# Optimization experiments

Measured on AMD Instinct MI355X. Metric: run time of the kernel, lower is better.

The kernel has to match this reference:

```python
import jax, jax.numpy as jnp
import numpy as np

H = 1024
B, S = 4, 2048
SCALE = 1.0 / np.sqrt(H)  # single-head: head_dim == hidden_dim


def setup_inputs() -> dict:
    key = jax.random.key(0)
    k1, k2, k3, k4 = jax.random.split(key, 4)
    inp = jax.random.normal(k1, (B, S, H), dtype=jnp.float32)
    # nn.Linear(h, h, bias=False) weights, stored [out, in]
    wq = jax.random.normal(k2, (H, H), dtype=jnp.float32) / np.sqrt(H)
    wk = jax.random.normal(k3, (H, H), dtype=jnp.float32) / np.sqrt(H)
    wv = jax.random.normal(k4, (H, H), dtype=jnp.float32) / np.sqrt(H)
    # causal mask, broadcast over batch: 1 = attend, 0 = masked
    attention_mask = jnp.broadcast_to(
        jnp.tril(jnp.ones((S, S), dtype=jnp.int32)), (B, S, S))
    return {"input": inp, "attention_mask": attention_mask,
            "wq": wq, "wk": wk, "wv": wv}


def reference(input, attention_mask, wq, wk, wv):
    # Linear: x @ W^T
    Q = jnp.einsum('bsh,oh->bso', input, wq)
    K = jnp.einsum('bsh,oh->bso', input, wk)
    V = jnp.einsum('bsh,oh->bso', input, wv)
    scores = jnp.einsum('bqh,bkh->bqk', Q, K) * SCALE  # [B,S,S]
    neg_inf = jnp.asarray(-jnp.inf, dtype=scores.dtype)
    scores = jnp.where(attention_mask == 0, neg_inf, scores)
    attn = jax.nn.softmax(scores, axis=-1)
    # dropout prob = 0.0 (eval): identity
    return jnp.einsum('bqk,bkh->bqh', attn, V)
```

## Files before the change

### kernel.cpp

```cpp
#include <hip/hip_runtime.h>
#include <hip/hip_bf16.h>
#include <stdint.h>

typedef __attribute__((ext_vector_type(8))) short short8;
typedef __attribute__((ext_vector_type(4))) float f32x4;
typedef __attribute__((ext_vector_type(4))) float fvec4;
typedef __attribute__((ext_vector_type(4))) unsigned short us4;

#define DEV static __device__ __forceinline__

constexpr int Hn = 1024;
constexpr int Bn = 4;
constexpr int Sn = 2048;
constexpr float SCALE_F = 0.03125f;
constexpr float LOG2E_F = 1.4426950408889634f;
constexpr float CEXP = SCALE_F * LOG2E_F;

DEV unsigned short f2bf(float f) {
  union { float f; unsigned u; } c; c.f = f;
  unsigned r = c.u + 0x7fffu + ((c.u >> 16) & 1u);
  return (unsigned short)(r >> 16);
}

DEV float bf2f(unsigned short b) {
  union { unsigned u; float f; } c; c.u = ((unsigned)b) << 16;
  return c.f;
}

DEV void gload16(const void* g, void* l) {
  __builtin_amdgcn_global_load_lds(
      (const __attribute__((address_space(1))) void*)g,
      (__attribute__((address_space(3))) void*)l, 16, 0, 0);
}

DEV void hw_barrier() { asm volatile("s_barrier" ::: "memory"); }

DEV int swz_wg(int bid, int n) {
  const int q = n >> 3, r = n & 7, x = bid & 7, o = bid >> 3;
  return (x < r ? x * (q + 1) : r * (q + 1) + (x - r) * q) + o;
}

__global__ __launch_bounds__(256) void cvt_kernel(
    const float* __restrict__ x, const float* __restrict__ wq,
    const float* __restrict__ wk, const float* __restrict__ wv,
    unsigned short* __restrict__ xb, unsigned short* __restrict__ wb) {
  const int NX4 = Bn * Sn * Hn / 4;
  const int NW4 = Hn * Hn / 4;
  const int total = NX4 + 3 * NW4;
  for (int i = blockIdx.x * 256 + threadIdx.x; i < total; i += gridDim.x * 256) {
    const fvec4* s; us4* d; int j;
    if (i < NX4)                { s = (const fvec4*)x;  d = (us4*)xb;             j = i; }
    else if (i < NX4 + NW4)     { s = (const fvec4*)wq; d = (us4*)wb;             j = i - NX4; }
    else if (i < NX4 + 2 * NW4) { s = (const fvec4*)wk; d = (us4*)(wb + Hn * Hn); j = i - NX4 - NW4; }
    else                        { s = (const fvec4*)wv; d = (us4*)(wb + 2 * Hn * Hn); j = i - NX4 - 2 * NW4; }
    fvec4 v = s[j];
    us4 o;
    o[0] = f2bf(v[0]); o[1] = f2bf(v[1]); o[2] = f2bf(v[2]); o[3] = f2bf(v[3]);
    d[j] = o;
  }
}

template <int MODE>
__global__ __launch_bounds__(512, 2) void gemm256_kernel(
    const unsigned short* __restrict__ A, int lda, int64_t a_bstride,
    const unsigned short* __restrict__ Bm, int ldb, int64_t b_bstride,
    unsigned short* __restrict__ C0, unsigned short* __restrict__ C1,
    int n_split, int ldc, int64_t c_bstride, int bm_mod, int K) {
  __shared__ __attribute__((aligned(16))) unsigned short LA[2][256 * 64];
  __shared__ __attribute__((aligned(16))) unsigned short LB[2][256 * 64];
  const int tid = threadIdx.x, lane = tid & 63, wave = tid >> 6;
  const int wr = wave >> 2, wc = wave & 3;

  int bm, bn;
  const unsigned short* Ab = A;
  const unsigned short* Bb = Bm;
  unsigned short* Cb = C0;
  if (MODE == 0) {
    const int wg = swz_wg(blockIdx.x, gridDim.x);
    bm = wg % bm_mod;
    bn = wg / bm_mod;
  } else {
    const int wg = swz_wg(blockIdx.x, gridDim.x);
    const int zl = wg / 36;
    const int t = wg - zl * 36;
    bm = (int)((sqrtf(8.f * t + 1.f) - 1.f) * 0.5f);
    if (bm * (bm + 1) / 2 > t) bm--;
    if ((bm + 1) * (bm + 2) / 2 <= t) bm++;
    bn = t - bm * (bm + 1) / 2;
    Ab += (int64_t)zl * a_bstride;
    Bb += (int64_t)zl * b_bstride;
    Cb += (int64_t)zl * c_bstride;
  }

  const int srow = wave * 32 + (lane >> 3);
  const int scol = (((lane & 7) ^ (lane >> 3)) << 3);
  const unsigned short* AgS = Ab + (int64_t)(bm * 256 + srow) * lda + scol;
  const unsigned short* BgS = Bb + (int64_t)(bn * 256 + srow) * ldb + scol;

  f32x4 zero = {0.f, 0.f, 0.f, 0.f};
  f32x4 acc[8][4];
#pragma unroll
  for (int m = 0; m < 8; m++)
#pragma unroll
    for (int n = 0; n < 4; n++) acc[m][n] = zero;

  auto stage = [&](int t, int buf) {
    char* la = (char*)LA[buf] + wave * 4096;
    char* lb = (char*)LB[buf] + wave * 4096;
    const int k0 = t << 6;
#pragma unroll
    for (int j = 0; j < 4; ++j) {
      gload16(AgS + (int64_t)(j * 8) * lda + k0, la + j * 1024);
      gload16(BgS + (int64_t)(j * 8) * ldb + k0, lb + j * 1024);
    }
  };

  const int nkt = K >> 6;
  const int ln15 = lane & 15;
  const int hi = (lane >> 4) * 16;
  const int sw = (ln15 & 7) << 4;

  stage(0, 0);
  for (int t = 0; t < nkt; ++t) {
    const int buf = t & 1;
    hw_barrier();
    if (t + 1 < nkt) {
      stage(t + 1, buf ^ 1);
      asm volatile("s_waitcnt vmcnt(8)" ::: "memory");
    } else {
      asm volatile("s_waitcnt vmcnt(0)" ::: "memory");
    }
    hw_barrier();
    __builtin_amdgcn_sched_barrier(0);

    const char* la = (const char*)LA[buf];
    const char* lb = (const char*)LB[buf];
#pragma unroll
    for (int qm = 0; qm < 2; ++qm) {
#pragma unroll
      for (int ks = 0; ks < 2; ++ks) {
        const int kb = (ks * 64 + hi) ^ sw;
        short8 a[4];
#pragma unroll
        for (int fr = 0; fr < 4; ++fr)
          a[fr] = *(const short8*)(la + (wr * 128 + qm * 64 + fr * 16 + ln15) * 128 + kb);
#pragma unroll
        for (int qn = 0; qn < 2; ++qn) {
          short8 b0 = *(const short8*)(lb + (wc * 64 + qn * 32 + ln15) * 128 + kb);
          short8 b1 = *(const short8*)(lb + (wc * 64 + qn * 32 + 16 + ln15) * 128 + kb);
          __builtin_amdgcn_s_setprio(1);
#pragma unroll
          for (int fr = 0; fr < 4; ++fr) {
            acc[qm * 4 + fr][qn * 2 + 0] =
                __builtin_amdgcn_mfma_f32_16x16x32_bf16(a[fr], b0, acc[qm * 4 + fr][qn * 2 + 0], 0, 0, 0);
            acc[qm * 4 + fr][qn * 2 + 1] =
                __builtin_amdgcn_mfma_f32_16x16x32_bf16(a[fr], b1, acc[qm * 4 + fr][qn * 2 + 1], 0, 0, 0);
          }
          __builtin_amdgcn_s_setprio(0);
        }
      }
    }
  }

  if (MODE == 0) {
#pragma unroll
    for (int n = 0; n < 4; n++) {
      int cc = bn * 256 + wc * 64 + n * 16;
      unsigned short* cb = Cb;
      if (cc >= n_split) { cb = C1; cc -= n_split; }
      cc += ln15;
#pragma unroll
      for (int m = 0; m < 8; m++) {
        const int r0 = bm * 256 + wr * 128 + m * 16 + ((lane >> 4) << 2);
#pragma unroll
        for (int j = 0; j < 4; j++)
          cb[(int64_t)(r0 + j) * ldc + cc] = f2bf(acc[m][n][j]);
      }
    }
  } else {
#pragma unroll
    for (int n = 0; n < 4; n++) {
      const int cc = bn * 256 + wc * 64 + n * 16 + ln15;
#pragma unroll
      for (int m = 0; m < 8; m++) {
        const int r0 = bm * 256 + wr * 128 + m * 16 + ((lane >> 4) << 2);
#pragma unroll
        for (int j = 0; j < 4; j++) {
          const int row = r0 + j;
          const float p = (cc <= row) ? __builtin_amdgcn_exp2f(acc[m][n][j] * CEXP) : 0.f;
          Cb[(int64_t)row * ldc + cc] = f2bf(p);
        }
      }
    }
  }
}

__global__ __launch_bounds__(256) void rowsum_kernel(
    const unsigned short* __restrict__ P, float* __restrict__ l, int b0, int nb) {
  const int lane = threadIdx.x & 63, wave = threadIdx.x >> 6;
  const int r = blockIdx.x * 4 + wave;
  if (r >= nb * Sn) return;
  const int bl = r >> 11;
  const int q = r & (Sn - 1);
  const unsigned short* Pr = P + (int64_t)bl * Sn * Sn + (int64_t)q * Sn;
  float s = 0.f;
  for (int base = lane * 8; base < Sn; base += 512) {
    const int rem = q + 1 - base;
    if (rem <= 0) continue;
    short8 v = *(const short8*)(Pr + base);
#pragma unroll
    for (int e = 0; e < 8; ++e)
      if (e < rem) s += bf2f((unsigned short)v[e]);
  }
#pragma unroll
  for (int m = 1; m < 64; m <<= 1) s += __shfl_xor(s, m);
  if (lane == 0) l[(int64_t)(b0 + bl) * Sn + q] = s;
}

__global__ __launch_bounds__(256) void pv_gemm_kernel(
    const unsigned short* __restrict__ P, int64_t p_zstride,
    const unsigned short* __restrict__ VTb,
    const float* __restrict__ l,
    float* __restrict__ Out, int b0, int nb) {
  const int per_bm = 8 * nb;
  const int w = blockIdx.x;
  const int bm = 15 - (w / per_bm);
  const int inner = w - (15 - bm) * per_bm;
  const int bn = inner & 7;
  const int zl = inner >> 3;
  const int b = b0 + zl;

  __shared__ __attribute__((aligned(16))) unsigned short As[2][128 * 32];
  __shared__ __attribute__((aligned(16))) unsigned short Bs[2][128 * 32];
  const int tid = threadIdx.x, lane = tid & 63, wave = tid >> 6;
  const int wr = wave >> 1, wc = wave & 1;

  const unsigned short* A = P + (int64_t)zl * p_zstride;
  const unsigned short* Ag = A + (int64_t)(bm * 128 + wave * 32 + (lane >> 2)) * Sn + (lane & 3) * 8;
  const unsigned short* Bg = VTb + (int64_t)(bn * 128 + wave * 32 + (lane >> 2)) * (Bn * Sn)
                             + (int64_t)b * Sn + (lane & 3) * 8;

  f32x4 zero = {0.f, 0.f, 0.f, 0.f};
  f32x4 acc[4][4];
#pragma unroll
  for (int m = 0; m < 4; m++)
#pragma unroll
    for (int n = 0; n < 4; n++) acc[m][n] = zero;

  auto stage = [&](int kt, int buf) {
    const int k0 = kt << 5;
    char* a = (char*)As[buf] + wave * 2048;
    char* b2 = (char*)Bs[buf] + wave * 2048;
    gload16(Ag + k0, a);
    gload16(Ag + k0 + 16 * Sn, a + 1024);
    gload16(Bg + k0, b2);
    gload16(Bg + k0 + (int64_t)16 * (Bn * Sn), b2 + 1024);
  };

  const int nkt = (bm + 1) * 4;
  stage(0, 0);
  __syncthreads();
  for (int kt = 0; kt < nkt; ++kt) {
    const int buf = kt & 1;
    if (kt + 1 < nkt) stage(kt + 1, buf ^ 1);
    const short* Ap = (const short*)As[buf];
    const short* Bp = (const short*)Bs[buf];
    const int ko = (lane >> 4) * 8;
    short8 af[4], bfv[4];
#pragma unroll
    for (int m = 0; m < 4; m++)
      af[m] = *(const short8*)(Ap + (wr * 64 + m * 16 + (lane & 15)) * 32 + ko);
#pragma unroll
    for (int n = 0; n < 4; n++)
      bfv[n] = *(const short8*)(Bp + (wc * 64 + n * 16 + (lane & 15)) * 32 + ko);
#pragma unroll
    for (int m = 0; m < 4; m++)
#pragma unroll
      for (int n = 0; n < 4; n++)
        acc[m][n] = __builtin_amdgcn_mfma_f32_16x16x32_bf16(af[m], bfv[n], acc[m][n], 0, 0, 0);
    __syncthreads();
  }

#pragma unroll
  for (int m = 0; m < 4; m++) {
    const int r0 = bm * 128 + wr * 64 + m * 16 + ((lane >> 4) << 2);
#pragma unroll
    for (int j = 0; j < 4; j++) {
      const int q = r0 + j;
      const float linv = 1.0f / l[(int64_t)b * Sn + q];
#pragma unroll
      for (int n = 0; n < 4; n++) {
        const int d = bn * 128 + wc * 64 + n * 16 + (lane & 15);
        Out[(int64_t)b * Sn * Hn + (int64_t)q * Hn + d] = acc[m][n][j] * linv;
      }
    }
  }
}

extern "C" void kernel_launch(void* const* d_in, const int* in_sizes, int n_in,
                              void* d_out, int out_size, void* d_ws, size_t ws_size,
                              hipStream_t stream) {
  const float* x  = (const float*)d_in[0];
  const float* wq = (const float*)d_in[2];
  const float* wk = (const float*)d_in[3];
  const float* wv = (const float*)d_in[4];
  float* out = (float*)d_out;
  char* ws = (char*)d_ws;

  const int64_t MiB = 1ll << 20;
  unsigned short* xb = (unsigned short*)(ws);
  unsigned short* wb = (unsigned short*)(ws + 16 * MiB);
  float* l           = (float*)(ws + 22 * MiB);
  unsigned short* Qb = (unsigned short*)(ws + 23 * MiB);
  unsigned short* Kb = (unsigned short*)(ws + 39 * MiB);
  unsigned short* VT = (unsigned short*)(ws + 55 * MiB);
  unsigned short* P  = (unsigned short*)(ws + 71 * MiB);

  cvt_kernel<<<2048, 256, 0, stream>>>(x, wq, wk, wv, xb, wb);
  gemm256_kernel<0><<<256, 512, 0, stream>>>(
      xb, 1024, 0, wb, 1024, 0, Qb, Kb, 1024, 1024, 0, 32, 1024);
  gemm256_kernel<0><<<128, 512, 0, stream>>>(
      wb + 2 * 1024 * 1024, 1024, 0, xb, 1024, 0, VT, VT, 1 << 30, 8192, 0, 4, 1024);

  int nb = 1;
  if (ws_size >= 103ull * MiB) nb = 4;
  else if (ws_size >= 87ull * MiB) nb = 2;
  for (int b0 = 0; b0 < Bn; b0 += nb) {
    gemm256_kernel<1><<<36 * nb, 512, 0, stream>>>(
        Qb + (int64_t)b0 * Sn * Hn, 1024, (int64_t)Sn * Hn,
        Kb + (int64_t)b0 * Sn * Hn, 1024, (int64_t)Sn * Hn,
        P, nullptr, 1 << 30, Sn, (int64_t)Sn * Sn, 8, 1024);
    rowsum_kernel<<<nb * 512, 256, 0, stream>>>(P, l, b0, nb);
    pv_gemm_kernel<<<16 * 8 * nb, 256, 0, stream>>>(
        P, (int64_t)Sn * Sn, VT, l, out, b0, nb);
  }
}
```

Baseline: 181.6 us.

## Fuse row-sum into QK GEMM, pack causal P tiles, restructure GEMM pipeline

The softmax row-sum is now computed in the QK^T epilogue through wave shuffles and atomicAdd, which removes the separate rowsum kernel and its re-read of P. P is stored as packed lower-triangular 128x128 tiles that reuse the freed xb region, so all batches run in a single launch instead of a workspace-dependent loop. The 256x256 GEMM main loop is rewritten to stage and consume A and B in halves with finer-grained barriers and waitcnts, overlapping loads with MFMA. PV loads use an XOR-swizzled LDS layout to reduce bank conflicts. The cost is atomics on the row sums, a zero-init folded into the convert kernel, and more complex synchronisation.

```diff
diff --git a/kernel.cpp b/kernel.cpp
--- a/kernel.cpp
+++ b/kernel.cpp
@@ -15,6 +15,7 @@
 constexpr float SCALE_F = 0.03125f;
 constexpr float LOG2E_F = 1.4426950408889634f;
 constexpr float CEXP = SCALE_F * LOG2E_F;
+constexpr int PTILES = 136;
 
 DEV unsigned short f2bf(float f) {
   union { float f; unsigned u; } c; c.f = f;
@@ -22,18 +23,15 @@
   return (unsigned short)(r >> 16);
 }
 
-DEV float bf2f(unsigned short b) {
-  union { unsigned u; float f; } c; c.u = ((unsigned)b) << 16;
-  return c.f;
-}
-
 DEV void gload16(const void* g, void* l) {
   __builtin_amdgcn_global_load_lds(
       (const __attribute__((address_space(1))) void*)g,
       (__attribute__((address_space(3))) void*)l, 16, 0, 0);
 }
 
-DEV void hw_barrier() { asm volatile("s_barrier" ::: "memory"); }
+#define VMCNT(n) asm volatile("s_waitcnt vmcnt(" #n ")" ::: "memory")
+#define LGKM0()  asm volatile("s_waitcnt lgkmcnt(0)" ::: "memory")
+#define BAR()    asm volatile("s_barrier" ::: "memory")
 
 DEV int swz_wg(int bid, int n) {
   const int q = n >> 3, r = n & 7, x = bid & 7, o = bid >> 3;
@@ -43,7 +41,12 @@
 __global__ __launch_bounds__(256) void cvt_kernel(
     const float* __restrict__ x, const float* __restrict__ wq,
     const float* __restrict__ wk, const float* __restrict__ wv,
-    unsigned short* __restrict__ xb, unsigned short* __restrict__ wb) {
+    unsigned short* __restrict__ xb, unsigned short* __restrict__ wb,
+    float* __restrict__ lz) {
+  if (blockIdx.x == 0) {
+    f32x4 z = {0.f, 0.f, 0.f, 0.f};
+    for (int i = threadIdx.x; i < Bn * Sn / 4; i += 256) ((f32x4*)lz)[i] = z;
+  }
   const int NX4 = Bn * Sn * Hn / 4;
   const int NW4 = Hn * Hn / 4;
   const int total = NX4 + 3 * NW4;
@@ -60,201 +63,218 @@
   }
 }
 
+#define MFMA16(H, V, B) do {                                                     \
+  __builtin_amdgcn_s_setprio(1);                                                 \
+  _Pragma("unroll") for (int m_ = 0; m_ < 4; m_++)                               \
+  _Pragma("unroll") for (int n_ = 0; n_ < 2; n_++)                               \
+  _Pragma("unroll") for (int ks_ = 0; ks_ < 2; ks_++)                            \
+    acc[H][V][m_][n_] = __builtin_amdgcn_mfma_f32_16x16x32_bf16(                 \
+        afr[m_][ks_], (B)[n_][ks_], acc[H][V][m_][n_], 0, 0, 0);                 \
+  __builtin_amdgcn_s_setprio(0);                                                 \
+  __builtin_amdgcn_sched_barrier(0);                                             \
+} while (0)
+
 template <int MODE>
 __global__ __launch_bounds__(512, 2) void gemm256_kernel(
     const unsigned short* __restrict__ A, int lda, int64_t a_bstride,
     const unsigned short* __restrict__ Bm, int ldb, int64_t b_bstride,
     unsigned short* __restrict__ C0, unsigned short* __restrict__ C1,
-    int n_split, int ldc, int64_t c_bstride, int bm_mod, int K) {
-  __shared__ __attribute__((aligned(16))) unsigned short LA[2][256 * 64];
-  __shared__ __attribute__((aligned(16))) unsigned short LB[2][256 * 64];
+    float* __restrict__ lsum, int n_split, int ldc, int bm_mod, int K) {
+  __shared__ __attribute__((aligned(16))) unsigned short LDSm[8][8192];
+  char* lds = (char*)LDSm;
   const int tid = threadIdx.x, lane = tid & 63, wave = tid >> 6;
   const int wr = wave >> 2, wc = wave & 3;
-
-  int bm, bn;
-  const unsigned short* Ab = A;
-  const unsigned short* Bb = Bm;
-  unsigned short* Cb = C0;
-  if (MODE == 0) {
-    const int wg = swz_wg(blockIdx.x, gridDim.x);
-    bm = wg % bm_mod;
-    bn = wg / bm_mod;
-  } else {
-    const int wg = swz_wg(blockIdx.x, gridDim.x);
-    const int zl = wg / 36;
+  const int ln15 = lane & 15, hi = lane >> 4;
+
+  int bm, bn, zl = 0;
+  const int wg = swz_wg(blockIdx.x, gridDim.x);
+  if (MODE == 0) { bm = wg % bm_mod; bn = wg / bm_mod; }
+  else {
+    zl = wg / 36;
     const int t = wg - zl * 36;
     bm = (int)((sqrtf(8.f * t + 1.f) - 1.f) * 0.5f);
     if (bm * (bm + 1) / 2 > t) bm--;
     if ((bm + 1) * (bm + 2) / 2 <= t) bm++;
     bn = t - bm * (bm + 1) / 2;
-    Ab += (int64_t)zl * a_bstride;
-    Bb += (int64_t)zl * b_bstride;
-    Cb += (int64_t)zl * c_bstride;
-  }
-
-  const int srow = wave * 32 + (lane >> 3);
-  const int scol = (((lane & 7) ^ (lane >> 3)) << 3);
-  const unsigned short* AgS = Ab + (int64_t)(bm * 256 + srow) * lda + scol;
-  const unsigned short* BgS = Bb + (int64_t)(bn * 256 + srow) * ldb + scol;
-
-  f32x4 zero = {0.f, 0.f, 0.f, 0.f};
-  f32x4 acc[8][4];
-#pragma unroll
-  for (int m = 0; m < 8; m++)
-#pragma unroll
-    for (int n = 0; n < 4; n++) acc[m][n] = zero;
-
-  auto stage = [&](int t, int buf) {
-    char* la = (char*)LA[buf] + wave * 4096;
-    char* lb = (char*)LB[buf] + wave * 4096;
-    const int k0 = t << 6;
-#pragma unroll
-    for (int j = 0; j < 4; ++j) {
-      gload16(AgS + (int64_t)(j * 8) * lda + k0, la + j * 1024);
-      gload16(BgS + (int64_t)(j * 8) * ldb + k0, lb + j * 1024);
-    }
-  };
+  }
+  const unsigned short* Ab = A + (int64_t)zl * a_bstride;
+  const unsigned short* Bb = Bm + (int64_t)zl * b_bstride;
+
+  const int srow = tid >> 3;
+  const int kch = ((tid & 7) ^ (srow & 7)) << 3;
+  const unsigned short* Ag = Ab + (int64_t)(bm * 256 + srow) * lda + kch;
+  const unsigned short* Bg = Bb + (int64_t)(bn * 256 + srow) * ldb + kch;
+  const int dst_off = tid * 16;
+
+  auto stageA = [&](int half, int t, int buf) {
+    const unsigned short* s = Ag + (int64_t)(half * 128) * lda + (t << 6);
+    char* d = lds + ((buf * 4 + half) << 14) + dst_off;
+    gload16(s, d);
+    gload16(s + (int64_t)64 * lda, d + 8192);
+  };
+  auto stageB = [&](int half, int t, int buf) {
+    const unsigned short* s = Bg + (int64_t)(half * 128) * ldb + (t << 6);
+    char* d = lds + ((buf * 4 + 2 + half) << 14) + dst_off;
+    gload16(s, d);
+    gload16(s + (int64_t)64 * ldb, d + 8192);
+  };
+  auto rdA = [&](int buf, int half, int rr, int ks) -> short8 {
+    return *(const short8*)(lds + ((buf * 4 + half) << 14) + rr * 128 +
+                            (((ks << 6) + (hi << 4)) ^ ((rr & 7) << 4)));
+  };
+  auto rdB = [&](int buf, int half, int rr, int ks) -> short8 {
+    return *(const short8*)(lds + ((buf * 4 + 2 + half) << 14) + rr * 128 +
+                            (((ks << 6) + (hi << 4)) ^ ((rr & 7) << 4)));
+  };
+
+  f32x4 acc[2][2][4][2];
+#pragma unroll
+  for (int h = 0; h < 2; h++)
+#pragma unroll
+    for (int v = 0; v < 2; v++)
+#pragma unroll
+      for (int m = 0; m < 4; m++)
+#pragma unroll
+        for (int n = 0; n < 2; n++) acc[h][v][m][n] = (f32x4){0.f, 0.f, 0.f, 0.f};
+
+  short8 afr[4][2], b0r[2][2], b1r[2][2];
+
+  stageA(0, 0, 0); stageB(0, 0, 0); stageB(1, 0, 0); stageA(1, 0, 0);
+  VMCNT(4);
+  BAR();
 
   const int nkt = K >> 6;
-  const int ln15 = lane & 15;
-  const int hi = (lane >> 4) * 16;
-  const int sw = (ln15 & 7) << 4;
-
-  stage(0, 0);
   for (int t = 0; t < nkt; ++t) {
-    const int buf = t & 1;
-    hw_barrier();
-    if (t + 1 < nkt) {
-      stage(t + 1, buf ^ 1);
-      asm volatile("s_waitcnt vmcnt(8)" ::: "memory");
-    } else {
-      asm volatile("s_waitcnt vmcnt(0)" ::: "memory");
-    }
-    hw_barrier();
-    __builtin_amdgcn_sched_barrier(0);
-
-    const char* la = (const char*)LA[buf];
-    const char* lb = (const char*)LB[buf];
-#pragma unroll
-    for (int qm = 0; qm < 2; ++qm) {
-#pragma unroll
-      for (int ks = 0; ks < 2; ++ks) {
-        const int kb = (ks * 64 + hi) ^ sw;
-        short8 a[4];
-#pragma unroll
-        for (int fr = 0; fr < 4; ++fr)
-          a[fr] = *(const short8*)(la + (wr * 128 + qm * 64 + fr * 16 + ln15) * 128 + kb);
-#pragma unroll
-        for (int qn = 0; qn < 2; ++qn) {
-          short8 b0 = *(const short8*)(lb + (wc * 64 + qn * 32 + ln15) * 128 + kb);
-          short8 b1 = *(const short8*)(lb + (wc * 64 + qn * 32 + 16 + ln15) * 128 + kb);
-          __builtin_amdgcn_s_setprio(1);
-#pragma unroll
-          for (int fr = 0; fr < 4; ++fr) {
-            acc[qm * 4 + fr][qn * 2 + 0] =
-                __builtin_amdgcn_mfma_f32_16x16x32_bf16(a[fr], b0, acc[qm * 4 + fr][qn * 2 + 0], 0, 0, 0);
-            acc[qm * 4 + fr][qn * 2 + 1] =
-                __builtin_amdgcn_mfma_f32_16x16x32_bf16(a[fr], b1, acc[qm * 4 + fr][qn * 2 + 1], 0, 0, 0);
+    const int buf = t & 1, nb2 = buf ^ 1;
+    const bool st = (t + 1 < nkt);
+#pragma unroll
+    for (int m = 0; m < 4; m++) {
+      afr[m][0] = rdA(buf, 0, wr * 64 + m * 16 + ln15, 0);
+      afr[m][1] = rdA(buf, 0, wr * 64 + m * 16 + ln15, 1);
+    }
+#pragma unroll
+    for (int n = 0; n < 2; n++) {
+      b0r[n][0] = rdB(buf, 0, wc * 32 + n * 16 + ln15, 0);
+      b0r[n][1] = rdB(buf, 0, wc * 32 + n * 16 + ln15, 1);
+    }
+    if (st) { stageA(0, t + 1, nb2); VMCNT(4); } else { VMCNT(2); }
+    BAR(); LGKM0(); __builtin_amdgcn_sched_barrier(0);
+    MFMA16(0, 0, b0r);
+    BAR();
+#pragma unroll
+    for (int n = 0; n < 2; n++) {
+      b1r[n][0] = rdB(buf, 1, wc * 32 + n * 16 + ln15, 0);
+      b1r[n][1] = rdB(buf, 1, wc * 32 + n * 16 + ln15, 1);
+    }
+    if (st) { stageB(0, t + 1, nb2); VMCNT(4); } else { VMCNT(0); }
+    BAR(); LGKM0(); __builtin_amdgcn_sched_barrier(0);
+    MFMA16(0, 1, b1r);
+    BAR();
+#pragma unroll
+    for (int m = 0; m < 4; m++) {
+      afr[m][0] = rdA(buf, 1, wr * 64 + m * 16 + ln15, 0);
+      afr[m][1] = rdA(buf, 1, wr * 64 + m * 16 + ln15, 1);
+    }
+    if (st) { stageB(1, t + 1, nb2); VMCNT(6); } else { VMCNT(0); }
+    BAR(); LGKM0(); __builtin_amdgcn_sched_barrier(0);
+    MFMA16(1, 0, b0r);
+    BAR();
+    if (st) { stageA(1, t + 1, nb2); VMCNT(4); } else { VMCNT(0); }
+    BAR();
+    MFMA16(1, 1, b1r);
+    BAR();
+  }
+
+  if (MODE == 0) {
+#pragma unroll
+    for (int h = 0; h < 2; h++)
+#pragma unroll
+      for (int v = 0; v < 2; v++)
+#pragma unroll
+        for (int n = 0; n < 2; n++) {
+          int cc = bn * 256 + v * 128 + wc * 32 + n * 16;
+          unsigned short* cb = C0;
+          if (cc >= n_split) { cb = C1; cc -= n_split; }
+          cc += ln15;
+#pragma unroll
+          for (int m = 0; m < 4; m++) {
+            const int r0 = bm * 256 + h * 128 + wr * 64 + m * 16 + hi * 4;
+#pragma unroll
+            for (int j = 0; j < 4; j++)
+              cb[(int64_t)(r0 + j) * ldc + cc] = f2bf(acc[h][v][m][n][j]);
           }
-          __builtin_amdgcn_s_setprio(0);
         }
-      }
-    }
-  }
-
-  if (MODE == 0) {
-#pragma unroll
-    for (int n = 0; n < 4; n++) {
-      int cc = bn * 256 + wc * 64 + n * 16;
-      unsigned short* cb = Cb;
-      if (cc >= n_split) { cb = C1; cc -= n_split; }
-      cc += ln15;
-#pragma unroll
-      for (int m = 0; m < 8; m++) {
-        const int r0 = bm * 256 + wr * 128 + m * 16 + ((lane >> 4) << 2);
-#pragma unroll
-        for (int j = 0; j < 4; j++)
-          cb[(int64_t)(r0 + j) * ldc + cc] = f2bf(acc[m][n][j]);
-      }
-    }
   } else {
-#pragma unroll
-    for (int n = 0; n < 4; n++) {
-      const int cc = bn * 256 + wc * 64 + n * 16 + ln15;
-#pragma unroll
-      for (int m = 0; m < 8; m++) {
-        const int r0 = bm * 256 + wr * 128 + m * 16 + ((lane >> 4) << 2);
+    unsigned short* Pb = C0 + (int64_t)zl * (PTILES * 16384);
+    float* lb = lsum + zl * Sn;
+#pragma unroll
+    for (int h = 0; h < 2; h++)
+#pragma unroll
+      for (int m = 0; m < 4; m++)
 #pragma unroll
         for (int j = 0; j < 4; j++) {
-          const int row = r0 + j;
-          const float p = (cc <= row) ? __builtin_amdgcn_exp2f(acc[m][n][j] * CEXP) : 0.f;
-          Cb[(int64_t)row * ldc + cc] = f2bf(p);
+          const int row = bm * 256 + h * 128 + wr * 64 + m * 16 + hi * 4 + j;
+          const int tq = row >> 7;
+          float s = 0.f;
+#pragma unroll
+          for (int v = 0; v < 2; v++)
+#pragma unroll
+            for (int n = 0; n < 2; n++) {
+              const int col = bn * 256 + v * 128 + wc * 32 + n * 16 + ln15;
+              const float p =
+                  (col <= row) ? __builtin_amdgcn_exp2f(acc[h][v][m][n][j] * CEXP) : 0.f;
+              s += p;
+              const int tk = col >> 7;
+              if (tk <= tq)
+                Pb[((int64_t)(tq * (tq + 1) / 2 + tk) << 14) + ((row & 127) << 7) +
+                   (col & 127)] = f2bf(p);
+            }
+          s += __shfl_xor(s, 1); s += __shfl_xor(s, 2);
+          s += __shfl_xor(s, 4); s += __shfl_xor(s, 8);
+          if (ln15 == 0) atomicAdd(&lb[row], s);
         }
-      }
-    }
-  }
-}
-
-__global__ __launch_bounds__(256) void rowsum_kernel(
-    const unsigned short* __restrict__ P, float* __restrict__ l, int b0, int nb) {
-  const int lane = threadIdx.x & 63, wave = threadIdx.x >> 6;
-  const int r = blockIdx.x * 4 + wave;
-  if (r >= nb * Sn) return;
-  const int bl = r >> 11;
-  const int q = r & (Sn - 1);
-  const unsigned short* Pr = P + (int64_t)bl * Sn * Sn + (int64_t)q * Sn;
-  float s = 0.f;
-  for (int base = lane * 8; base < Sn; base += 512) {
-    const int rem = q + 1 - base;
-    if (rem <= 0) continue;
-    short8 v = *(const short8*)(Pr + base);
-#pragma unroll
-    for (int e = 0; e < 8; ++e)
-      if (e < rem) s += bf2f((unsigned short)v[e]);
-  }
-#pragma unroll
-  for (int m = 1; m < 64; m <<= 1) s += __shfl_xor(s, m);
-  if (lane == 0) l[(int64_t)(b0 + bl) * Sn + q] = s;
+  }
 }
 
 __global__ __launch_bounds__(256) void pv_gemm_kernel(
-    const unsigned short* __restrict__ P, int64_t p_zstride,
+    const unsigned short* __restrict__ Pp,
     const unsigned short* __restrict__ VTb,
     const float* __restrict__ l,
-    float* __restrict__ Out, int b0, int nb) {
-  const int per_bm = 8 * nb;
+    float* __restrict__ Out) {
   const int w = blockIdx.x;
-  const int bm = 15 - (w / per_bm);
-  const int inner = w - (15 - bm) * per_bm;
+  const int bm = 15 - (w >> 5);
+  const int inner = w & 31;
   const int bn = inner & 7;
-  const int zl = inner >> 3;
-  const int b = b0 + zl;
+  const int b = inner >> 3;
 
   __shared__ __attribute__((aligned(16))) unsigned short As[2][128 * 32];
   __shared__ __attribute__((aligned(16))) unsigned short Bs[2][128 * 32];
   const int tid = threadIdx.x, lane = tid & 63, wave = tid >> 6;
   const int wr = wave >> 1, wc = wave & 1;
-
-  const unsigned short* A = P + (int64_t)zl * p_zstride;
-  const unsigned short* Ag = A + (int64_t)(bm * 128 + wave * 32 + (lane >> 2)) * Sn + (lane & 3) * 8;
-  const unsigned short* Bg = VTb + (int64_t)(bn * 128 + wave * 32 + (lane >> 2)) * (Bn * Sn)
-                             + (int64_t)b * Sn + (lane & 3) * 8;
-
-  f32x4 zero = {0.f, 0.f, 0.f, 0.f};
+  const int ln15 = lane & 15, hi = lane >> 4;
+
+  const int arow = wave * 32 + (lane >> 2);
+  const int aswz = (((lane & 3) ^ ((lane >> 2) & 3)) << 3);
+  const unsigned short* Abase = Pp + (int64_t)b * (PTILES * 16384) +
+      ((int64_t)(bm * (bm + 1) / 2) << 14) + (arow << 7) + aswz;
+  const unsigned short* Bg = VTb + (int64_t)(bn * 128 + arow) * (Bn * Sn) +
+      (int64_t)b * Sn + aswz;
+
   f32x4 acc[4][4];
 #pragma unroll
   for (int m = 0; m < 4; m++)
 #pragma unroll
-    for (int n = 0; n < 4; n++) acc[m][n] = zero;
+    for (int n = 0; n < 4; n++) acc[m][n] = (f32x4){0.f, 0.f, 0.f, 0.f};
 
   auto stage = [&](int kt, int buf) {
-    const int k0 = kt << 5;
+    const unsigned short* a_src = Abase + ((int64_t)(kt >> 2) << 14) + (kt & 3) * 32;
+    const unsigned short* b_src = Bg + kt * 32;
     char* a = (char*)As[buf] + wave * 2048;
-    char* b2 = (char*)Bs[buf] + wave * 2048;
-    gload16(Ag + k0, a);
-    gload16(Ag + k0 + 16 * Sn, a + 1024);
-    gload16(Bg + k0, b2);
-    gload16(Bg + k0 + (int64_t)16 * (Bn * Sn), b2 + 1024);
+    char* bl = (char*)Bs[buf] + wave * 2048;
+    gload16(a_src, a);
+    gload16(a_src + 2048, a + 1024);
+    gload16(b_src, bl);
+    gload16(b_src + (int64_t)16 * (Bn * Sn), bl + 1024);
   };
 
   const int nkt = (bm + 1) * 4;
@@ -263,16 +283,19 @@
   for (int kt = 0; kt < nkt; ++kt) {
     const int buf = kt & 1;
     if (kt + 1 < nkt) stage(kt + 1, buf ^ 1);
-    const short* Ap = (const short*)As[buf];
-    const short* Bp = (const short*)Bs[buf];
-    const int ko = (lane >> 4) * 8;
+    const char* Ap = (const char*)As[buf];
+    const char* Bp = (const char*)Bs[buf];
     short8 af[4], bfv[4];
 #pragma unroll
-    for (int m = 0; m < 4; m++)
-      af[m] = *(const short8*)(Ap + (wr * 64 + m * 16 + (lane & 15)) * 32 + ko);
-#pragma unroll
-    for (int n = 0; n < 4; n++)
-      bfv[n] = *(const short8*)(Bp + (wc * 64 + n * 16 + (lane & 15)) * 32 + ko);
+    for (int m = 0; m < 4; m++) {
+      const int rr = wr * 64 + m * 16 + ln15;
+      af[m] = *(const short8*)(Ap + rr * 64 + ((hi ^ (rr & 3)) << 4));
+    }
+#pragma unroll
+    for (int n = 0; n < 4; n++) {
+      const int rr = wc * 64 + n * 16 + ln15;
+      bfv[n] = *(const short8*)(Bp + rr * 64 + ((hi ^ (rr & 3)) << 4));
+    }
 #pragma unroll
     for (int m = 0; m < 4; m++)
 #pragma unroll
@@ -283,14 +306,14 @@
 
 #pragma unroll
   for (int m = 0; m < 4; m++) {
-    const int r0 = bm * 128 + wr * 64 + m * 16 + ((lane >> 4) << 2);
+    const int r0 = bm * 128 + wr * 64 + m * 16 + hi * 4;
 #pragma unroll
     for (int j = 0; j < 4; j++) {
       const int q = r0 + j;
       const float linv = 1.0f / l[(int64_t)b * Sn + q];
 #pragma unroll
       for (int n = 0; n < 4; n++) {
-        const int d = bn * 128 + wc * 64 + n * 16 + (lane & 15);
+        const int d = bn * 128 + wc * 64 + n * 16 + ln15;
         Out[(int64_t)b * Sn * Hn + (int64_t)q * Hn + d] = acc[m][n][j] * linv;
       }
     }
@@ -310,28 +333,19 @@
   const int64_t MiB = 1ll << 20;
   unsigned short* xb = (unsigned short*)(ws);
   unsigned short* wb = (unsigned short*)(ws + 16 * MiB);
+  unsigned short* Pp = (unsigned short*)(ws);
   float* l           = (float*)(ws + 22 * MiB);
   unsigned short* Qb = (unsigned short*)(ws + 23 * MiB);
   unsigned short* Kb = (unsigned short*)(ws + 39 * MiB);
   unsigned short* VT = (unsigned short*)(ws + 55 * MiB);
-  unsigned short* P  = (unsigned short*)(ws + 71 * MiB);
-
-  cvt_kernel<<<2048, 256, 0, stream>>>(x, wq, wk, wv, xb, wb);
+
+  cvt_kernel<<<2048, 256, 0, stream>>>(x, wq, wk, wv, xb, wb, l);
   gemm256_kernel<0><<<256, 512, 0, stream>>>(
-      xb, 1024, 0, wb, 1024, 0, Qb, Kb, 1024, 1024, 0, 32, 1024);
+      xb, 1024, 0, wb, 1024, 0, Qb, Kb, nullptr, 1024, 1024, 32, 1024);
   gemm256_kernel<0><<<128, 512, 0, stream>>>(
-      wb + 2 * 1024 * 1024, 1024, 0, xb, 1024, 0, VT, VT, 1 << 30, 8192, 0, 4, 1024);
-
-  int nb = 1;
-  if (ws_size >= 103ull * MiB) nb = 4;
-  else if (ws_size >= 87ull * MiB) nb = 2;
-  for (int b0 = 0; b0 < Bn; b0 += nb) {
-    gemm256_kernel<1><<<36 * nb, 512, 0, stream>>>(
-        Qb + (int64_t)b0 * Sn * Hn, 1024, (int64_t)Sn * Hn,
-        Kb + (int64_t)b0 * Sn * Hn, 1024, (int64_t)Sn * Hn,
-        P, nullptr, 1 << 30, Sn, (int64_t)Sn * Sn, 8, 1024);
-    rowsum_kernel<<<nb * 512, 256, 0, stream>>>(P, l, b0, nb);
-    pv_gemm_kernel<<<16 * 8 * nb, 256, 0, stream>>>(
-        P, (int64_t)Sn * Sn, VT, l, out, b0, nb);
-  }
-}
+      wb + 2 * 1024 * 1024, 1024, 0, xb, 1024, 0, VT, VT, nullptr, 1 << 30, 8192, 4, 1024);
+  gemm256_kernel<1><<<144, 512, 0, stream>>>(
+      Qb, 1024, (int64_t)Sn * Hn, Kb, 1024, (int64_t)Sn * Hn,
+      Pp, nullptr, l, 1 << 30, 0, 0, 1024);
+  pv_gemm_kernel<<<512, 256, 0, stream>>>(Pp, VT, l, out);
+}
```

After: 169.5 us. 6.7% less time.
